# Optimization experiments

Hardware: AMD Instinct MI355X
Metric: run time of the kernel (lower is better)

The kernel has to match this reference:

```python
import jax, jax.numpy as jnp
import numpy as np

DIM = 768
B, S = 16, 1024
EPS = 1e-5


def setup_inputs() -> dict:
    key = jax.random.key(0)
    ks = jax.random.split(key, 13)
    std = 1.0 / np.sqrt(DIM)
    inp = {
        "x_A": jax.random.normal(ks[0], (B, S, DIM), jnp.float32),
        "x_B": jax.random.normal(ks[1], (B, S, DIM), jnp.float32),
        "x_C": jax.random.normal(ks[2], (B, S, DIM), jnp.float32),
        "W_q": jax.random.normal(ks[3], (DIM, DIM), jnp.float32) * std,
        "b_q": jax.random.normal(ks[4], (DIM,), jnp.float32) * std,
        "W_k": jax.random.normal(ks[5], (DIM, DIM), jnp.float32) * std,
        "b_k": jax.random.normal(ks[6], (DIM,), jnp.float32) * std,
        "W_v": jax.random.normal(ks[7], (DIM, DIM), jnp.float32) * std,
        "b_v": jax.random.normal(ks[8], (DIM,), jnp.float32) * std,
        "gamma": jnp.ones((DIM,), jnp.float32),
        "beta": jnp.zeros((DIM,), jnp.float32),
        "W_fc": jax.random.normal(ks[9], (DIM, DIM), jnp.float32) * std,
        "b_fc": jax.random.normal(ks[10], (DIM,), jnp.float32) * std,
    }
    return inp


def _linear(x, W, b):
    # torch nn.Linear: x @ W.T + b
    return jnp.einsum('bsd,ed->bse', x, W) + b


def _layernorm(x, gamma, beta):
    mu = jnp.mean(x, axis=-1, keepdims=True)
    var = jnp.mean((x - mu) ** 2, axis=-1, keepdims=True)
    return (x - mu) * jax.lax.rsqrt(var + EPS) * gamma + beta


def reference(x_A, x_B, x_C, W_q, b_q, W_k, b_k, W_v, b_v, gamma, beta, W_fc, b_fc):
    scale = 1.0 / jnp.sqrt(jnp.float32(DIM))
    Q = _linear(x_C, W_q, b_q)
    K_A = _linear(x_A, W_k, b_k)
    K_B = _linear(x_B, W_k, b_k)
    V_A = _linear(x_A, W_v, b_v)
    V_B = _linear(x_B, W_v, b_v)
    attn_A = jax.nn.softmax(jnp.einsum('bqd,bkd->bqk', Q, K_A) * scale, axis=-1)
    attn_B = jax.nn.softmax(jnp.einsum('bqd,bkd->bqk', Q, K_B) * scale, axis=-1)
    interp_A = jnp.einsum('bqk,bkd->bqd', attn_A, V_A)
    interp_B = jnp.einsum('bqk,bkd->bqd', attn_B, V_B)
    h = _layernorm(interp_A + interp_B + x_C, gamma, beta)
    return _linear(h, W_fc, b_fc)
```

## Files before the change

kernel.cpp:

```cpp
#include <hip/hip_runtime.h>

#define DIMV 768
#define BATCH 16
#define SEQ 1024
#define LN_EPS 1e-5f

typedef __attribute__((ext_vector_type(8))) short bf16x8;
typedef __attribute__((ext_vector_type(4))) float f32x4;
typedef unsigned short ushort_t;

__device__ __forceinline__ unsigned short f2bf(float f) {
    unsigned u = __float_as_uint(f);
    u = (u + 0x7FFFu + ((u >> 16) & 1u)) >> 16;
    return (unsigned short)u;
}

__global__ __launch_bounds__(256) void gemm_bf16_nt(
    const ushort_t* __restrict__ A, const ushort_t* __restrict__ B,
    const float* __restrict__ bias, void* __restrict__ Cout,
    int K, int lda, int ldb, int ldc, float scale, int mode,
    long long sAz, long long sBz, long long sCz)
{
    int bx = blockIdx.x, by = blockIdx.y, bz = blockIdx.z;
    {
        const unsigned Z = gridDim.z;
        if (Z > 1) {
            const unsigned nx = gridDim.x, ny = gridDim.y;
            const unsigned nxy = nx * ny;
            const unsigned lid = ((unsigned)bz * ny + (unsigned)by) * nx + (unsigned)bx;
            unsigned r;
            if ((Z & 7u) == 0u) {
                const unsigned c  = lid & 7u;
                const unsigned rp = lid >> 3;
                bz = (int)(c + 8u * (rp / nxy));
                r  = rp % nxy;
            } else {
                bz = (int)(lid % Z);
                r  = lid / Z;
            }
            bx = (int)(r % nx);
            by = (int)(r / nx);
        }
    }

    A += (long long)bz * sAz;
    B += (long long)bz * sBz;
    float*    Cf = (float*)Cout    + ((mode == 0 || mode == 3) ? (long long)bz * sCz : 0);
    ushort_t* Ch = (ushort_t*)Cout + ((mode == 1 || mode == 2) ? (long long)bz * sCz : 0);

    __shared__ ushort_t As[3][128 * 32];
    __shared__ ushort_t Bs[3][128 * 32];

    const int t    = threadIdx.x;
    const int wave = t >> 6;
    const int lane = t & 63;
    const int quad = lane >> 4;
    const int lr   = lane & 15;
    const int wy   = wave >> 1;
    const int wx   = wave & 1;

    const int m0 = by * 128;
    const int n0 = bx * 128;

    const ushort_t* Abase = A + (long long)m0 * lda;
    const ushort_t* Bbase = B + (long long)n0 * ldb;

    auto issue = [&](int k0, int slot) {
        #pragma unroll
        for (int i = 0; i < 2; ++i) {
            const int idx = t + 256 * i;
            const int r   = idx >> 2;
            const int c   = (idx & 3) * 8;
            __builtin_amdgcn_global_load_lds(
                (const __attribute__((address_space(1))) unsigned int*)(Abase + (long long)r * lda + k0 + c),
                (__attribute__((address_space(3))) unsigned int*)&As[slot][idx * 8], 16, 0, 0);
            __builtin_amdgcn_global_load_lds(
                (const __attribute__((address_space(1))) unsigned int*)(Bbase + (long long)r * ldb + k0 + c),
                (__attribute__((address_space(3))) unsigned int*)&Bs[slot][idx * 8], 16, 0, 0);
        }
    };

    f32x4 acc[4][4] = {};

    const int NK = K >> 5;
    issue(0, 0);
    int cur = 0, nxt = 1;
    for (int ki = 0; ki < NK; ++ki) {
        const int kn = (ki + 1 < NK) ? (ki + 1) << 5 : 0;
        issue(kn, nxt);
        asm volatile("s_waitcnt vmcnt(4)" ::: "memory");
        asm volatile("s_barrier" ::: "memory");

        const ushort_t* as = &As[cur][0];
        const ushort_t* bs = &Bs[cur][0];
        bf16x8 af[4], bfr[4];
        #pragma unroll
        for (int i = 0; i < 4; ++i) {
            const int row = wy * 64 + i * 16 + lr;
            af[i] = *(const bf16x8*)&as[row * 32 + quad * 8];
        }
        #pragma unroll
        for (int j = 0; j < 4; ++j) {
            const int row = wx * 64 + j * 16 + lr;
            bfr[j] = *(const bf16x8*)&bs[row * 32 + quad * 8];
        }
        #pragma unroll
        for (int i = 0; i < 4; ++i)
            #pragma unroll
            for (int j = 0; j < 4; ++j)
                acc[i][j] = __builtin_amdgcn_mfma_f32_16x16x32_bf16(
                    af[i], bfr[j], acc[i][j], 0, 0, 0);

        cur = nxt;
        nxt = (nxt == 2) ? 0 : nxt + 1;
    }

    #pragma unroll
    for (int j = 0; j < 4; ++j) {
        const int n = n0 + wx * 64 + j * 16 + lr;
        const float bv = bias ? bias[n] : 0.0f;
        #pragma unroll
        for (int i = 0; i < 4; ++i) {
            #pragma unroll
            for (int r = 0; r < 4; ++r) {
                const int m = m0 + wy * 64 + i * 16 + quad * 4 + r;
                const float val = acc[i][j][r] * scale + bv;
                if (mode == 0) {
                    Cf[(long long)m * ldc + n] = val;
                } else if (mode == 3) {
                    Cf[(long long)m * ldc + n] += val;
                } else if (mode == 1) {
                    Ch[(long long)m * ldc + n] = f2bf(val);
                } else {
                    const int b = m >> 10, s = m & 1023;
                    Ch[(long long)b * (DIMV * SEQ) + (long long)n * SEQ + s] = f2bf(val);
                }
            }
        }
    }
}

__global__ __launch_bounds__(256) void f32_to_bf16(
    const float* __restrict__ in, ushort_t* __restrict__ out)
{
    const long long i = ((long long)blockIdx.x * 256 + threadIdx.x) * 4;
    float4 v = *reinterpret_cast<const float4*>(in + i);
    ushort4 o;
    o.x = f2bf(v.x); o.y = f2bf(v.y); o.z = f2bf(v.z); o.w = f2bf(v.w);
    *reinterpret_cast<ushort4*>(out + i) = o;
}

__global__ __launch_bounds__(256) void softmax_inplace(float* __restrict__ S)
{
    float* s = S + (long long)blockIdx.x * SEQ;
    const int t = threadIdx.x;
    __shared__ float red[256];

    float4 v = *reinterpret_cast<const float4*>(&s[t * 4]);
    float mx = fmaxf(fmaxf(v.x, v.y), fmaxf(v.z, v.w));
    red[t] = mx;
    __syncthreads();
    for (int st = 128; st > 0; st >>= 1) {
        if (t < st) red[t] = fmaxf(red[t], red[t + st]);
        __syncthreads();
    }
    mx = red[0];
    __syncthreads();

    v.x = __expf(v.x - mx); v.y = __expf(v.y - mx);
    v.z = __expf(v.z - mx); v.w = __expf(v.w - mx);
    red[t] = v.x + v.y + v.z + v.w;
    __syncthreads();
    for (int st = 128; st > 0; st >>= 1) {
        if (t < st) red[t] += red[t + st];
        __syncthreads();
    }
    const float inv = 1.0f / red[0];

    ushort4 o;
    o.x = f2bf(v.x * inv); o.y = f2bf(v.y * inv);
    o.z = f2bf(v.z * inv); o.w = f2bf(v.w * inv);
    *reinterpret_cast<ushort4*>((ushort_t*)s + t * 4) = o;
}

__global__ __launch_bounds__(256) void add_layernorm(
    const float* __restrict__ ACC, const float* __restrict__ xC,
    const float* __restrict__ gamma, const float* __restrict__ beta,
    ushort_t* __restrict__ H)
{
    const long long row = blockIdx.x;
    const float* a = ACC + row * DIMV;
    const float* x = xC  + row * DIMV;
    ushort_t*    h = H   + row * DIMV;
    const int t = threadIdx.x;

    __shared__ float r1[256];
    __shared__ float r2[256];

    float vals[3];
    float s = 0.f, ss = 0.f;
    #pragma unroll
    for (int i = 0; i < 3; ++i) {
        const int j = t + i * 256;
        float v = a[j] + x[j];
        vals[i] = v;
        s += v; ss += v * v;
    }
    r1[t] = s; r2[t] = ss;
    __syncthreads();
    for (int st = 128; st > 0; st >>= 1) {
        if (t < st) { r1[t] += r1[t + st]; r2[t] += r2[t + st]; }
        __syncthreads();
    }
    const float mu  = r1[0] * (1.0f / DIMV);
    const float var = r2[0] * (1.0f / DIMV) - mu * mu;
    const float inv = rsqrtf(var + LN_EPS);

    #pragma unroll
    for (int i = 0; i < 3; ++i) {
        const int j = t + i * 256;
        h[j] = f2bf((vals[i] - mu) * inv * gamma[j] + beta[j]);
    }
}

extern "C" void kernel_launch(void* const* d_in, const int* in_sizes, int n_in,
                              void* d_out, int out_size, void* d_ws, size_t ws_size,
                              hipStream_t stream)
{
    const float* xA    = (const float*)d_in[0];
    const float* xB    = (const float*)d_in[1];
    const float* xC    = (const float*)d_in[2];
    const float* Wq    = (const float*)d_in[3];
    const float* bq    = (const float*)d_in[4];
    const float* Wk    = (const float*)d_in[5];
    const float* bk    = (const float*)d_in[6];
    const float* Wv    = (const float*)d_in[7];
    const float* bv    = (const float*)d_in[8];
    const float* gamma = (const float*)d_in[9];
    const float* beta  = (const float*)d_in[10];
    const float* Wfc   = (const float*)d_in[11];
    const float* bfc   = (const float*)d_in[12];
    float* out = (float*)d_out;

    const long long eW   = (long long)DIMV * DIMV;
    const long long perB = (long long)SEQ * DIMV;
    const long long perP = (long long)SEQ * SEQ;

    const long long wBytes        = 4 * eW * 2;
    const long long perBatchBytes = 14 * perB + 4 * perP;

    long long Cmax = ((long long)ws_size - wBytes) / perBatchBytes;
    if (Cmax > BATCH) Cmax = BATCH;
    if (Cmax < 1)     Cmax = 1;
    const int nChunks = (int)((BATCH + Cmax - 1) / Cmax);
    const int CbStd   = (BATCH + nChunks - 1) / nChunks;

    char* cur = (char*)d_ws;
    ushort_t* Wqb  = (ushort_t*)cur; cur += eW * 2;
    ushort_t* Wkb  = (ushort_t*)cur; cur += eW * 2;
    ushort_t* Wvb  = (ushort_t*)cur; cur += eW * 2;
    ushort_t* Wfcb = (ushort_t*)cur; cur += eW * 2;
    char* chunkBase = cur;

    const float scale = 0.03608439182435161f;

    f32_to_bf16<<<(int)(eW / 1024), 256, 0, stream>>>(Wq,  Wqb);
    f32_to_bf16<<<(int)(eW / 1024), 256, 0, stream>>>(Wk,  Wkb);
    f32_to_bf16<<<(int)(eW / 1024), 256, 0, stream>>>(Wv,  Wvb);
    f32_to_bf16<<<(int)(eW / 1024), 256, 0, stream>>>(Wfc, Wfcb);

    for (int b0 = 0; b0 < BATCH; b0 += CbStd) {
        const int Cb = (b0 + CbStd <= BATCH) ? CbStd : (BATCH - b0);
        const long long off = (long long)b0 * perB;

        char* p = chunkBase;
        ushort_t* xABb = (ushort_t*)p;
        float*    ACC  = (float*)p;    p += (long long)Cb * 4 * perB;
        float*    Sf   = (float*)p;
        ushort_t* xCb  = (ushort_t*)p; p += (long long)Cb * 4 * perP;
        ushort_t* Qb   = (ushort_t*)p; p += (long long)Cb * 2 * perB;
        ushort_t* Kb   = (ushort_t*)p; p += (long long)Cb * 4 * perB;
        ushort_t* Vtb  = (ushort_t*)p; p += (long long)Cb * 4 * perB;

        dim3 gq (DIMV / 128, Cb * (SEQ / 128), 1);
        dim3 gkv(DIMV / 128, 2 * Cb * (SEQ / 128), 1);
        dim3 gsc(SEQ / 128, SEQ / 128, Cb);
        dim3 gpv(DIMV / 128, SEQ / 128, Cb);
        const int gcv = (int)((long long)Cb * perB / 1024);

        f32_to_bf16<<<gcv, 256, 0, stream>>>(xC + off, xCb);
        gemm_bf16_nt<<<gq, 256, 0, stream>>>(xCb, Wqb, bq, Qb,
            DIMV, DIMV, DIMV, DIMV, 1.f, 1, 0, 0, 0);
        f32_to_bf16<<<gcv, 256, 0, stream>>>(xA + off, xABb);
        f32_to_bf16<<<gcv, 256, 0, stream>>>(xB + off, xABb + (long long)Cb * perB);
        gemm_bf16_nt<<<gkv, 256, 0, stream>>>(xABb, Wkb, bk, Kb,
            DIMV, DIMV, DIMV, DIMV, 1.f, 1, 0, 0, 0);
        gemm_bf16_nt<<<gkv, 256, 0, stream>>>(xABb, Wvb, bv, Vtb,
            DIMV, DIMV, DIMV, DIMV, 1.f, 2, 0, 0, 0);

        gemm_bf16_nt<<<gsc, 256, 0, stream>>>(Qb, Kb, nullptr, Sf,
            DIMV, DIMV, DIMV, SEQ, scale, 0, perB, perB, perP);
        softmax_inplace<<<Cb * SEQ, 256, 0, stream>>>(Sf);
        gemm_bf16_nt<<<gpv, 256, 0, stream>>>((const ushort_t*)Sf, Vtb, nullptr, ACC,
            SEQ, 2 * SEQ, SEQ, DIMV, 1.f, 0, 2 * perP, perB, perB);

        gemm_bf16_nt<<<gsc, 256, 0, stream>>>(Qb, Kb + (long long)Cb * perB, nullptr, Sf,
            DIMV, DIMV, DIMV, SEQ, scale, 0, perB, perB, perP);
        softmax_inplace<<<Cb * SEQ, 256, 0, stream>>>(Sf);
        gemm_bf16_nt<<<gpv, 256, 0, stream>>>((const ushort_t*)Sf, Vtb + (long long)Cb * perB, nullptr, ACC,
            SEQ, 2 * SEQ, SEQ, DIMV, 1.f, 3, 2 * perP, perB, perB);

        add_layernorm<<<Cb * SEQ, 256, 0, stream>>>(ACC, xC + off, gamma, beta, Qb);

        gemm_bf16_nt<<<gq, 256, 0, stream>>>(Qb, Wfcb, bfc, out + off,
            DIMV, DIMV, DIMV, DIMV, 1.f, 0, 0, 0, 0);
    }
}
```

Measured before the change: 746.8 us.

## Fuse K and V projections into one GEMM and add XCD-aware block remap

The separate K and V projection launches are merged into one GEMM over a concatenated [Wk;Wv] bf16 weight. A new epilogue mode writes the first half of the columns as row-major K and the second half transposed as V^T. This reads the activations once instead of twice and removes a launch. Separately, 2D grids whose block count is a multiple of 8 get their block ids remapped so that neighbouring tiles land on the same XCD, aiming for better L2 reuse. The cost is extra branching in the epilogue.

After: 714.3 us. -4.4%, faster.

```diff
diff --git a/kernel.cpp b/kernel.cpp
--- a/kernel.cpp
+++ b/kernel.cpp
@@ -17,15 +17,16 @@
 
 __global__ __launch_bounds__(256) void gemm_bf16_nt(
     const ushort_t* __restrict__ A, const ushort_t* __restrict__ B,
-    const float* __restrict__ bias, void* __restrict__ Cout,
+    const float* __restrict__ bias, const float* __restrict__ bias2,
+    void* __restrict__ Cout, void* __restrict__ Cout2,
     int K, int lda, int ldb, int ldc, float scale, int mode,
     long long sAz, long long sBz, long long sCz)
 {
     int bx = blockIdx.x, by = blockIdx.y, bz = blockIdx.z;
     {
-        const unsigned Z = gridDim.z;
+        const unsigned Z  = gridDim.z;
+        const unsigned nx = gridDim.x, ny = gridDim.y;
         if (Z > 1) {
-            const unsigned nx = gridDim.x, ny = gridDim.y;
             const unsigned nxy = nx * ny;
             const unsigned lid = ((unsigned)bz * ny + (unsigned)by) * nx + (unsigned)bx;
             unsigned r;
@@ -40,13 +41,22 @@
             }
             bx = (int)(r % nx);
             by = (int)(r / nx);
+        } else {
+            const unsigned nwg = nx * ny;
+            if ((nwg & 7u) == 0u) {
+                const unsigned lid = (unsigned)by * nx + (unsigned)bx;
+                const unsigned nl  = (lid & 7u) * (nwg >> 3) + (lid >> 3);
+                bx = (int)(nl % nx);
+                by = (int)(nl / nx);
+            }
         }
     }
 
     A += (long long)bz * sAz;
     B += (long long)bz * sBz;
-    float*    Cf = (float*)Cout    + ((mode == 0 || mode == 3) ? (long long)bz * sCz : 0);
-    ushort_t* Ch = (ushort_t*)Cout + ((mode == 1 || mode == 2) ? (long long)bz * sCz : 0);
+    float*    Cf  = (float*)Cout    + ((mode == 0 || mode == 3) ? (long long)bz * sCz : 0);
+    ushort_t* Ch  = (ushort_t*)Cout + ((mode == 1 || mode == 2) ? (long long)bz * sCz : 0);
+    ushort_t* Ch2 = (ushort_t*)Cout2;
 
     __shared__ ushort_t As[3][128 * 32];
     __shared__ ushort_t Bs[3][128 * 32];
@@ -118,7 +128,9 @@
     #pragma unroll
     for (int j = 0; j < 4; ++j) {
         const int n = n0 + wx * 64 + j * 16 + lr;
-        const float bv = bias ? bias[n] : 0.0f;
+        float bv;
+        if (mode == 4) bv = (n < DIMV) ? bias[n] : bias2[n - DIMV];
+        else           bv = bias ? bias[n] : 0.0f;
         #pragma unroll
         for (int i = 0; i < 4; ++i) {
             #pragma unroll
@@ -131,9 +143,16 @@
                     Cf[(long long)m * ldc + n] += val;
                 } else if (mode == 1) {
                     Ch[(long long)m * ldc + n] = f2bf(val);
-                } else {
+                } else if (mode == 2) {
                     const int b = m >> 10, s = m & 1023;
                     Ch[(long long)b * (DIMV * SEQ) + (long long)n * SEQ + s] = f2bf(val);
+                } else {
+                    if (n < DIMV) {
+                        Ch[(long long)m * ldc + n] = f2bf(val);
+                    } else {
+                        const int b = m >> 10, s = m & 1023;
+                        Ch2[(long long)b * (DIMV * SEQ) + (long long)(n - DIMV) * SEQ + s] = f2bf(val);
+                    }
                 }
             }
         }
@@ -257,16 +276,15 @@
 
     char* cur = (char*)d_ws;
     ushort_t* Wqb  = (ushort_t*)cur; cur += eW * 2;
-    ushort_t* Wkb  = (ushort_t*)cur; cur += eW * 2;
-    ushort_t* Wvb  = (ushort_t*)cur; cur += eW * 2;
+    ushort_t* Wkvb = (ushort_t*)cur; cur += 2 * eW * 2;
     ushort_t* Wfcb = (ushort_t*)cur; cur += eW * 2;
     char* chunkBase = cur;
 
     const float scale = 0.03608439182435161f;
 
     f32_to_bf16<<<(int)(eW / 1024), 256, 0, stream>>>(Wq,  Wqb);
-    f32_to_bf16<<<(int)(eW / 1024), 256, 0, stream>>>(Wk,  Wkb);
-    f32_to_bf16<<<(int)(eW / 1024), 256, 0, stream>>>(Wv,  Wvb);
+    f32_to_bf16<<<(int)(eW / 1024), 256, 0, stream>>>(Wk,  Wkvb);
+    f32_to_bf16<<<(int)(eW / 1024), 256, 0, stream>>>(Wv,  Wkvb + eW);
     f32_to_bf16<<<(int)(eW / 1024), 256, 0, stream>>>(Wfc, Wfcb);
 
     for (int b0 = 0; b0 < BATCH; b0 += CbStd) {
@@ -282,37 +300,35 @@
         ushort_t* Kb   = (ushort_t*)p; p += (long long)Cb * 4 * perB;
         ushort_t* Vtb  = (ushort_t*)p; p += (long long)Cb * 4 * perB;
 
-        dim3 gq (DIMV / 128, Cb * (SEQ / 128), 1);
-        dim3 gkv(DIMV / 128, 2 * Cb * (SEQ / 128), 1);
-        dim3 gsc(SEQ / 128, SEQ / 128, Cb);
-        dim3 gpv(DIMV / 128, SEQ / 128, Cb);
+        dim3 gq  (DIMV / 128, Cb * (SEQ / 128), 1);
+        dim3 gkv (2 * DIMV / 128, 2 * Cb * (SEQ / 128), 1);
+        dim3 gsc (SEQ / 128, SEQ / 128, Cb);
+        dim3 gpv (DIMV / 128, SEQ / 128, Cb);
         const int gcv = (int)((long long)Cb * perB / 1024);
 
         f32_to_bf16<<<gcv, 256, 0, stream>>>(xC + off, xCb);
-        gemm_bf16_nt<<<gq, 256, 0, stream>>>(xCb, Wqb, bq, Qb,
+        gemm_bf16_nt<<<gq, 256, 0, stream>>>(xCb, Wqb, bq, nullptr, Qb, nullptr,
             DIMV, DIMV, DIMV, DIMV, 1.f, 1, 0, 0, 0);
         f32_to_bf16<<<gcv, 256, 0, stream>>>(xA + off, xABb);
         f32_to_bf16<<<gcv, 256, 0, stream>>>(xB + off, xABb + (long long)Cb * perB);
-        gemm_bf16_nt<<<gkv, 256, 0, stream>>>(xABb, Wkb, bk, Kb,
-            DIMV, DIMV, DIMV, DIMV, 1.f, 1, 0, 0, 0);
-        gemm_bf16_nt<<<gkv, 256, 0, stream>>>(xABb, Wvb, bv, Vtb,
-            DIMV, DIMV, DIMV, DIMV, 1.f, 2, 0, 0, 0);
-
-        gemm_bf16_nt<<<gsc, 256, 0, stream>>>(Qb, Kb, nullptr, Sf,
+        gemm_bf16_nt<<<gkv, 256, 0, stream>>>(xABb, Wkvb, bk, bv, Kb, Vtb,
+            DIMV, DIMV, DIMV, DIMV, 1.f, 4, 0, 0, 0);
+
+        gemm_bf16_nt<<<gsc, 256, 0, stream>>>(Qb, Kb, nullptr, nullptr, Sf, nullptr,
             DIMV, DIMV, DIMV, SEQ, scale, 0, perB, perB, perP);
         softmax_inplace<<<Cb * SEQ, 256, 0, stream>>>(Sf);
-        gemm_bf16_nt<<<gpv, 256, 0, stream>>>((const ushort_t*)Sf, Vtb, nullptr, ACC,
+        gemm_bf16_nt<<<gpv, 256, 0, stream>>>((const ushort_t*)Sf, Vtb, nullptr, nullptr, ACC, nullptr,
             SEQ, 2 * SEQ, SEQ, DIMV, 1.f, 0, 2 * perP, perB, perB);
 
-        gemm_bf16_nt<<<gsc, 256, 0, stream>>>(Qb, Kb + (long long)Cb * perB, nullptr, Sf,
+        gemm_bf16_nt<<<gsc, 256, 0, stream>>>(Qb, Kb + (long long)Cb * perB, nullptr, nullptr, Sf, nullptr,
             DIMV, DIMV, DIMV, SEQ, scale, 0, perB, perB, perP);
         softmax_inplace<<<Cb * SEQ, 256, 0, stream>>>(Sf);
-        gemm_bf16_nt<<<gpv, 256, 0, stream>>>((const ushort_t*)Sf, Vtb + (long long)Cb * perB, nullptr, ACC,
+        gemm_bf16_nt<<<gpv, 256, 0, stream>>>((const ushort_t*)Sf, Vtb + (long long)Cb * perB, nullptr, nullptr, ACC, nullptr,
             SEQ, 2 * SEQ, SEQ, DIMV, 1.f, 3, 2 * perP, perB, perB);
 
         add_layernorm<<<Cb * SEQ, 256, 0, stream>>>(ACC, xC + off, gamma, beta, Qb);
 
-        gemm_bf16_nt<<<gq, 256, 0, stream>>>(Qb, Wfcb, bfc, out + off,
+        gemm_bf16_nt<<<gq, 256, 0, stream>>>(Qb, Wfcb, bfc, nullptr, out + off, nullptr,
             DIMV, DIMV, DIMV, DIMV, 1.f, 0, 0, 0, 0);
     }
 }
```
